# Performance work log

Measured on AMD Instinct MI355X. Metric: run time of the kernel, lower is better.

Reference implementation:

```python
import jax, jax.numpy as jnp
import numpy as np
import math

D_MODEL = 1024
D_STATE = 16
D_CONV = 4
EXPAND = 2
D_INNER = EXPAND * D_MODEL
DT_RANK = 64
BATCH = 4
SEQ_LEN = 2048


def setup_inputs() -> dict:
    key = jax.random.key(0)
    ks = jax.random.split(key, 10)
    hidden_states = jax.random.normal(ks[0], (BATCH, SEQ_LEN, D_MODEL), jnp.float32)
    in_proj_w = jax.random.normal(ks[1], (D_MODEL, 2 * D_INNER), jnp.float32) * (D_MODEL ** -0.5)
    conv_w = jax.random.normal(ks[2], (D_INNER, D_CONV), jnp.float32) * (D_CONV ** -0.5)
    conv_b = jnp.zeros((D_INNER,), jnp.float32)
    x_proj_w = jax.random.normal(ks[3], (D_INNER, DT_RANK + 2 * D_STATE), jnp.float32) * (D_INNER ** -0.5)
    dt_init_std = DT_RANK ** -0.5
    dt_proj_w = jax.random.uniform(ks[4], (DT_RANK, D_INNER), jnp.float32, -dt_init_std, dt_init_std)
    # inverse-softplus init of dt bias: dt ~ logUniform(dt_min, dt_max)
    dt_min, dt_max, dt_floor = 0.001, 0.1, 1e-4
    dt = jnp.exp(jax.random.uniform(ks[5], (D_INNER,), jnp.float32) * (math.log(dt_max) - math.log(dt_min)) + math.log(dt_min))
    dt = jnp.clip(dt, dt_floor, None)
    dt_proj_b = dt + jnp.log(-jnp.expm1(-dt))
    A = jnp.tile(jnp.arange(1, D_STATE + 1, dtype=jnp.float32)[None, :], (D_INNER, 1))
    A_log = jnp.log(A)
    D = jnp.ones((D_INNER,), jnp.float32)
    out_proj_w = jax.random.normal(ks[6], (D_INNER, D_MODEL), jnp.float32) * (D_INNER ** -0.5)
    return {
        "hidden_states": hidden_states,
        "in_proj_w": in_proj_w,
        "conv_w": conv_w,
        "conv_b": conv_b,
        "x_proj_w": x_proj_w,
        "dt_proj_w": dt_proj_w,
        "dt_proj_b": dt_proj_b,
        "A_log": A_log,
        "D": D,
        "out_proj_w": out_proj_w,
    }


def _mamba_forward(hidden_states, in_proj_w, conv_w, conv_b, x_proj_w, dt_proj_w, dt_proj_b, A_log, D, out_proj_w):
    b, L, _ = hidden_states.shape
    d_state = A_log.shape[1]
    dt_rank = dt_proj_w.shape[0]
    K = conv_w.shape[1]

    xz = hidden_states @ in_proj_w                     # (b, L, 2*d_inner)
    x, z = jnp.split(xz, 2, axis=-1)                   # each (b, L, d_inner)

    # causal depthwise conv1d (padding = K-1, truncated to L)
    x_pad = jnp.pad(x, ((0, 0), (K - 1, 0), (0, 0)))
    x = sum(x_pad[:, k:k + L, :] * conv_w[:, k] for k in range(K)) + conv_b
    x = jax.nn.silu(x)

    x_dbl = x @ x_proj_w                               # (b, L, dt_rank + 2*d_state)
    dt, B, C = jnp.split(x_dbl, [dt_rank, dt_rank + d_state], axis=-1)
    dt = jax.nn.softplus(dt @ dt_proj_w + dt_proj_b)   # (b, L, d_inner)
    A = -jnp.exp(A_log)                                # (d_inner, d_state)

    def step(h, inp):
        x_t, dt_t, B_t, C_t = inp                      # (b,d), (b,d), (b,n), (b,n)
        dA = jnp.exp(A[None] * dt_t[..., None])        # (b, d, n)
        h = dA * h + dt_t[..., None] * B_t[:, None, :] * x_t[..., None]
        y_t = jnp.einsum('bdn,bn->bd', h, C_t) + D * x_t
        return h, y_t

    h0 = jnp.zeros((b, x.shape[-1], d_state), x.dtype)
    xs = (x.transpose(1, 0, 2), dt.transpose(1, 0, 2), B.transpose(1, 0, 2), C.transpose(1, 0, 2))
    _, ys = jax.lax.scan(step, h0, xs)                 # ys: (L, b, d_inner)
    y = ys.transpose(1, 0, 2) * jax.nn.silu(z)
    return y @ out_proj_w                              # (b, L, d_model)


def reference(hidden_states, in_proj_w, conv_w, conv_b, x_proj_w, dt_proj_w, dt_proj_b, A_log, D, out_proj_w):
    return _mamba_forward(hidden_states, in_proj_w, conv_w, conv_b, x_proj_w, dt_proj_w, dt_proj_b, A_log, D, out_proj_w)
```

## Files before the change

### kernel.cpp

```cpp
#include <hip/hip_runtime.h>
#include <hip/hip_bf16.h>


#define DM 1024
#define DS 16
#define DC 4
#define DI 2048
#define DR 64
#define NB 4
#define SL 2048
#define NTOK (NB*SL)
#define XDBL_W (DR + 2*DS)
#define CONV_R 8

typedef __hip_bfloat16 bf16;
typedef unsigned short u16;
typedef __attribute__((ext_vector_type(8))) short s8v;
typedef __attribute__((ext_vector_type(4))) float f4v;
typedef __attribute__((ext_vector_type(4))) unsigned short us4;

__device__ __forceinline__ float b2f(bf16 v) { return __bfloat162float(v); }
__device__ __forceinline__ bf16  f2b(float v) { return __float2bfloat16(v); }
__device__ __forceinline__ u16 f2u(float x) {
    union { bf16 h; u16 s; } u; u.h = f2b(x); return u.s;
}
__device__ __forceinline__ float u2f(u16 s) {
    union { bf16 h; u16 s; } u; u.s = s; return b2f(u.h);
}

__device__ __forceinline__ bool sniff_bf16(const void* Dones) {
    return ((const u16*)Dones)[0] == 0x3F80u;
}

__device__ __forceinline__ float softplus_fast(float v) {
    return fmaxf(v, 0.f) + __logf(1.f + __expf(-fabsf(v)));
}

template<int MODE>
__device__ __forceinline__ float ld(const void* p, size_t i, bool bf) {
    if (MODE == 0) return b2f(((const bf16*)p)[i]);
    if (MODE == 1) return ((const float*)p)[i];
    return bf ? b2f(((const bf16*)p)[i]) : ((const float*)p)[i];
}
template<int MODE>
__device__ __forceinline__ void st(void* p, size_t i, bool bf, float v) {
    if (MODE == 0)      { ((bf16*)p)[i] = f2b(v); }
    else if (MODE == 1) { ((float*)p)[i] = v; }
    else { if (bf) ((bf16*)p)[i] = f2b(v); else ((float*)p)[i] = v; }
}

template<int CM>
__device__ __forceinline__ void cstore(void* C, void* C2, size_t m, int n,
                                       int ldc, bool bf, float v) {
    if (CM == 3) {
        if (n < DR) ((bf16*)C2)[m * DR + n] = f2b(v);
        else        ((float*)C)[m * (2 * DS) + (n - DR)] = v;
    } else {
        st<CM>(C, m * (size_t)ldc + n, bf, v);
    }
}

#define AS1 __attribute__((address_space(1)))
#define AS3 __attribute__((address_space(3)))
__device__ __forceinline__ void gload_lds16(const void* g, void* l) {
    __builtin_amdgcn_global_load_lds((const AS1 unsigned int*)g,
                                     (AS3 unsigned int*)l, 16, 0, 0);
}

__global__ __launch_bounds__(256) void cast_bf16_kernel(
    const void* __restrict__ src, bf16* __restrict__ dst,
    const void* __restrict__ sniff)
{
    const bool bf = sniff_bf16(sniff);
    const size_t i = ((size_t)blockIdx.x * 256 + threadIdx.x) * 4;
    if (bf) {
        *(us4*)((u16*)dst + i) = *(const us4*)((const u16*)src + i);
    } else {
        const f4v f = *(const f4v*)((const float*)src + i);
        us4 o; o.x = f2u(f.x); o.y = f2u(f.y); o.z = f2u(f.z); o.w = f2u(f.w);
        *(us4*)((u16*)dst + i) = o;
    }
}

__global__ __launch_bounds__(256) void transpose_w(
    const void* __restrict__ w, bf16* __restrict__ wt,
    int K, int N, const void* __restrict__ sniff)
{
    const bool bf = sniff_bf16(sniff);
    __shared__ float t[32][33];
    const int tx = threadIdx.x & 31, ty = threadIdx.x >> 5;
    const int n0 = blockIdx.x * 32, k0 = blockIdx.y * 32;
    #pragma unroll
    for (int i = 0; i < 4; i++) {
        int k = k0 + ty + i * 8, n = n0 + tx;
        t[ty + i * 8][tx] = (n < N) ? ld<2>(w, (size_t)k * N + n, bf) : 0.f;
    }
    __syncthreads();
    #pragma unroll
    for (int i = 0; i < 4; i++) {
        int n = n0 + ty + i * 8, k = k0 + tx;
        wt[(size_t)n * K + k] = f2b(t[tx][ty + i * 8]);
    }
}

template<int BM, int BN, int WM, int WN, int CM>
__global__ __launch_bounds__(WM*WN*64, 2) void gemm_big(
    const bf16* __restrict__ A, int lda,
    const bf16* __restrict__ Bt,
    void* __restrict__ C, int ldc, int K,
    const void* __restrict__ sniff)
{
    constexpr int NT  = WM * WN;
    constexpr int NTH = NT * 64;
    constexpr int WAVE_M = BM / WM, WAVE_N = BN / WN;
    constexpr int MR = WAVE_M / 16, NR = WAVE_N / 16, MR2 = MR / 2;
    constexpr int CH_ROWS = NTH / 8;
    constexpr int ACH = BM / CH_ROWS;
    constexpr int BCH = BN / CH_ROWS;

    const bool bf = sniff_bf16(sniff);
    __shared__ short Asm[2][BM * 64];
    __shared__ short Bsm[2][BN * 64];

    const int tid = threadIdx.x, lane = tid & 63, wave = tid >> 6;
    const int wm = wave / WN, wn = wave % WN;
    const int ll = lane & 15, qd = lane >> 4;
    const int m0 = blockIdx.x * BM, n0 = blockIdx.y * BN;

    const int s_r  = tid >> 3;
    const int s_cb = ((tid & 7) * 16) ^ ((s_r & 7) << 4);

    const char* Ab = (const char*)A;
    const char* Bb = (const char*)Bt;

    f4v acc[MR][NR];
    #pragma unroll
    for (int i = 0; i < MR; i++)
        #pragma unroll
        for (int j = 0; j < NR; j++) acc[i][j] = (f4v){0.f, 0.f, 0.f, 0.f};

    #pragma unroll
    for (int c = 0; c < ACH; c++)
        gload_lds16(Ab + (((size_t)(m0 + c * CH_ROWS + s_r) * lda) << 1) + s_cb,
                    (char*)&Asm[0][0] + (c * NTH + tid) * 16);
    #pragma unroll
    for (int c = 0; c < BCH; c++)
        gload_lds16(Bb + (((size_t)(n0 + c * CH_ROWS + s_r) * K) << 1) + s_cb,
                    (char*)&Bsm[0][0] + (c * NTH + tid) * 16);
    asm volatile("s_waitcnt vmcnt(0)" ::: "memory");
    __builtin_amdgcn_sched_barrier(0);
    __builtin_amdgcn_s_barrier();

    const int NTILE = K >> 6;
    for (int t = 0; t < NTILE; ++t) {
        const int cur = t & 1, nxt = cur ^ 1;
        const int kk = (t + 1) << 6;
        const bool more = (t + 1 < NTILE);
        const char* Ac = (const char*)&Asm[cur][0];
        const char* Bc = (const char*)&Bsm[cur][0];
        #pragma unroll
        for (int p = 0; p < 4; ++p) {
            const int kh = p >> 1, mh = p & 1;
            const int kb = kh * 64;
            s8v af[MR2], bv[NR];
            #pragma unroll
            for (int i = 0; i < MR2; i++) {
                const int row = wm * WAVE_M + (mh * MR2 + i) * 16 + ll;
                af[i] = *(const s8v*)(Ac + (size_t)row * 128
                                        + ((kb + qd * 16) ^ ((ll & 7) << 4)));
            }
            #pragma unroll
            for (int j = 0; j < NR; j++) {
                const int row = wn * WAVE_N + j * 16 + ll;
                bv[j] = *(const s8v*)(Bc + (size_t)row * 128
                                        + ((kb + qd * 16) ^ ((ll & 7) << 4)));
            }
            if (p == 0 && more) {
                #pragma unroll
                for (int c = 0; c < ACH; c++)
                    gload_lds16(Ab + (((size_t)(m0 + c * CH_ROWS + s_r) * lda + kk) << 1) + s_cb,
                                (char*)&Asm[nxt][0] + (c * NTH + tid) * 16);
            }
            if (p == 1 && more) {
                #pragma unroll
                for (int c = 0; c < BCH; c++)
                    gload_lds16(Bb + (((size_t)(n0 + c * CH_ROWS + s_r) * K + kk) << 1) + s_cb,
                                (char*)&Bsm[nxt][0] + (c * NTH + tid) * 16);
            }
            __builtin_amdgcn_sched_barrier(0);
            __builtin_amdgcn_s_barrier();
            asm volatile("s_waitcnt lgkmcnt(0)" ::: "memory");
            __builtin_amdgcn_sched_barrier(0);
            __builtin_amdgcn_s_setprio(1);
            #pragma unroll
            for (int i = 0; i < MR2; i++)
                #pragma unroll
                for (int j = 0; j < NR; j++)
                    acc[mh * MR2 + i][j] = __builtin_amdgcn_mfma_f32_16x16x32_bf16(
                        af[i], bv[j], acc[mh * MR2 + i][j], 0, 0, 0);
            __builtin_amdgcn_s_setprio(0);
            if (p == 3) {
                asm volatile("s_waitcnt vmcnt(0)" ::: "memory");
            }
            __builtin_amdgcn_sched_barrier(0);
            __builtin_amdgcn_s_barrier();
        }
    }

    #pragma unroll
    for (int i = 0; i < MR; i++) {
        #pragma unroll
        for (int j = 0; j < NR; j++) {
            const int col = n0 + wn * WAVE_N + j * 16 + ll;
            #pragma unroll
            for (int r = 0; r < 4; r++) {
                const int row = m0 + wm * WAVE_M + i * 16 + qd * 4 + r;
                st<CM>(C, (size_t)row * ldc + col, bf, acc[i][j][r]);
            }
        }
    }
}

template<int CM, int EPI>
__global__ __launch_bounds__(256) void gemm_mfma(
    const bf16* __restrict__ A, int lda,
    const bf16* __restrict__ Bt,
    void* __restrict__ C, void* __restrict__ C2, int ldc,
    int M, int N, int K,
    const void* __restrict__ bias,
    const void* __restrict__ sniff)
{
    const bool bf = sniff_bf16(sniff);
    __shared__ short As[128 * 32];
    __shared__ short Bs[128 * 32];

    const int tid  = threadIdx.x;
    const int lane = tid & 63;
    const int wave = tid >> 6;
    const int wm = (wave & 1) * 64;
    const int wn = (wave >> 1) * 64;
    const int m0 = blockIdx.x * 128;
    const int n0 = blockIdx.y * 128;
    const int ll = lane & 15;
    const int qd = lane >> 4;

    const int srow  = lane >> 2;
    const int skoff = (lane & 3) * 8;

    const short* Ag = (const short*)A;
    const short* Bg = (const short*)Bt;
    char* AsB = (char*)As + wave * 2048 + lane * 16;
    char* BsB = (char*)Bs + wave * 2048 + lane * 16;
    const size_t a_row = (size_t)(m0 + wave * 32 + srow);
    const size_t b_row = (size_t)(n0 + wave * 32 + srow);

    f4v acc[4][4];
    #pragma unroll
    for (int i = 0; i < 4; i++)
        #pragma unroll
        for (int j = 0; j < 4; j++)
            acc[i][j] = (f4v){0.f, 0.f, 0.f, 0.f};

    for (int k0 = 0; k0 < K; k0 += 32) {
        gload_lds16(Ag + a_row * lda + k0 + skoff,            AsB);
        gload_lds16(Ag + (a_row + 16) * lda + k0 + skoff,     AsB + 1024);
        gload_lds16(Bg + b_row * K + k0 + skoff,              BsB);
        gload_lds16(Bg + (b_row + 16) * K + k0 + skoff,       BsB + 1024);
        __syncthreads();

        s8v af[4], bfr[4];
        #pragma unroll
        for (int s = 0; s < 4; s++)
            af[s] = *(const s8v*)&As[(wm + s * 16 + ll) * 32 + qd * 8];
        #pragma unroll
        for (int s = 0; s < 4; s++)
            bfr[s] = *(const s8v*)&Bs[(wn + s * 16 + ll) * 32 + qd * 8];
        #pragma unroll
        for (int i = 0; i < 4; i++)
            #pragma unroll
            for (int j = 0; j < 4; j++)
                acc[i][j] = __builtin_amdgcn_mfma_f32_16x16x32_bf16(
                    af[i], bfr[j], acc[i][j], 0, 0, 0);
        __syncthreads();
    }

    #pragma unroll
    for (int sn = 0; sn < 4; sn++) {
        const int cn = n0 + wn + sn * 16 + ll;
        if (cn >= N) continue;
        float bvv = 0.f;
        if (EPI == 1) bvv = ld<2>(bias, cn, bf);
        #pragma unroll
        for (int sm = 0; sm < 4; sm++) {
            #pragma unroll
            for (int r = 0; r < 4; r++) {
                const int cm = m0 + wm + sm * 16 + qd * 4 + r;
                float v = acc[sm][sn][r];
                if (EPI == 1) v = softplus_fast(v + bvv);
                cstore<CM>(C, C2, (size_t)cm, cn, ldc, bf, v);
            }
        }
    }
}

template<int AM, int CM, int EPI>
__global__ __launch_bounds__(256) void gemm_kernel(
    const void* __restrict__ A, int lda,
    const void* __restrict__ B, size_t bbase, int ldb,
    void* __restrict__ C, void* __restrict__ C2, int ldc,
    int M, int N, int K,
    const void* __restrict__ bias,
    const void* __restrict__ sniff)
{
    const bool bf = sniff_bf16(sniff);
    const int BM = 64, BN = 64, BK = 16;
    __shared__ float Asm[BK][BM + 4];
    __shared__ float Bsm[BK][BN + 4];

    const int tid = threadIdx.x;
    const int m0 = blockIdx.x * BM;
    const int n0 = blockIdx.y * BN;
    const int tx = tid % 16;
    const int ty = tid / 16;
    const int a_k = tid % BK;
    const int a_m = tid / BK;
    const int b_n = tid % BN;
    const int b_k = tid / BN;

    float acc[4][4] = {};

    for (int k0 = 0; k0 < K; k0 += BK) {
        #pragma unroll
        for (int i = 0; i < 4; i++) {
            int m = m0 + a_m + i * 16;
            float v = 0.f;
            if (m < M) v = ld<AM>(A, (size_t)m * lda + (k0 + a_k), bf);
            Asm[a_k][a_m + i * 16] = v;
        }
        #pragma unroll
        for (int i = 0; i < 4; i++) {
            int kk = b_k + i * 4;
            int n = n0 + b_n;
            float v = 0.f;
            if (n < N) v = ld<2>(B, bbase + (size_t)(k0 + kk) * ldb + n, bf);
            Bsm[kk][b_n] = v;
        }
        __syncthreads();
        #pragma unroll
        for (int kk = 0; kk < BK; kk++) {
            float av[4], bv[4];
            #pragma unroll
            for (int i = 0; i < 4; i++) av[i] = Asm[kk][ty * 4 + i];
            #pragma unroll
            for (int j = 0; j < 4; j++) bv[j] = Bsm[kk][tx * 4 + j];
            #pragma unroll
            for (int i = 0; i < 4; i++)
                #pragma unroll
                for (int j = 0; j < 4; j++)
                    acc[i][j] += av[i] * bv[j];
        }
        __syncthreads();
    }
    #pragma unroll
    for (int i = 0; i < 4; i++) {
        int m = m0 + ty * 4 + i;
        if (m >= M) continue;
        #pragma unroll
        for (int j = 0; j < 4; j++) {
            int n = n0 + tx * 4 + j;
            if (n >= N) continue;
            float v = acc[i][j];
            if (EPI == 1) {
                v += ld<2>(bias, n, bf);
                v = softplus_fast(v);
            }
            cstore<CM>(C, C2, (size_t)m, n, ldc, bf, v);
        }
    }
}

__global__ __launch_bounds__(256) void conv_silu_kernel(
    const bf16* __restrict__ xg, const void* __restrict__ w,
    const void* __restrict__ bias, bf16* __restrict__ xc,
    const void* __restrict__ sniff)
{
    const bool bf = sniff_bf16(sniff);
    const int c  = blockIdx.x * 256 + threadIdx.x;
    const int r0 = blockIdx.y * CONV_R;
    const int l0 = r0 % SL;

    float w0, w1, w2, w3;
    if (bf) {
        const us4 wv = *(const us4*)((const u16*)w + (size_t)c * 4);
        w0 = u2f(wv.x); w1 = u2f(wv.y); w2 = u2f(wv.z); w3 = u2f(wv.w);
    } else {
        const f4v wv = *(const f4v*)((const float*)w + (size_t)c * 4);
        w0 = wv.x; w1 = wv.y; w2 = wv.z; w3 = wv.w;
    }
    const float bs = ld<2>(bias, c, bf);

    float xm3 = (l0 >= 3) ? b2f(xg[(size_t)(r0 - 3) * DI + c]) : 0.f;
    float xm2 = (l0 >= 2) ? b2f(xg[(size_t)(r0 - 2) * DI + c]) : 0.f;
    float xm1 = (l0 >= 1) ? b2f(xg[(size_t)(r0 - 1) * DI + c]) : 0.f;

    #pragma unroll
    for (int i = 0; i < CONV_R; i++) {
        const size_t row = (size_t)(r0 + i);
        const float x0 = b2f(xg[row * DI + c]);
        const float acc = bs + w0 * xm3 + w1 * xm2 + w2 * xm1 + w3 * x0;
        const float s = acc / (1.f + __expf(-acc));
        xc[row * DI + c] = f2b(s);
        xm3 = xm2; xm2 = xm1; xm1 = x0;
    }
}

__global__ __launch_bounds__(256) void scan_pass1(
    const bf16* __restrict__ xc, const bf16* __restrict__ dt,
    const float* __restrict__ bc,
    const void* __restrict__ A_log, const void* __restrict__ Dones,
    float* __restrict__ P, float* __restrict__ Q, int nch)
{
    const bool bf = sniff_bf16(Dones);
    const int d = blockIdx.x * 256 + threadIdx.x;
    const int c = blockIdx.y;
    const int b = blockIdx.z;
    const int T = SL / nch;

    float a[DS], Pp[DS], Qq[DS];
    bool lad = true;
    #pragma unroll
    for (int n = 0; n < DS; n++) {
        a[n] = -__expf(ld<2>(A_log, (size_t)d * DS + n, bf));
        Pp[n] = 1.f; Qq[n] = 0.f;
        lad = lad && (fabsf(a[n] - (n + 1) * a[0]) < 1e-3f);
    }

    const size_t base = (size_t)b * SL + (size_t)c * T;
    if (lad) {
        const float a0 = a[0];
        for (int i = 0; i < T; i++) {
            const size_t row = base + i;
            const float xv  = b2f(xc[row * DI + d]);
            const float dtv = b2f(dt[row * DI + d]);
            const float dtx = dtv * xv;
            const float* Bv = bc + row * (2 * DS);
            const float r = __expf(a0 * dtv);
            float cur = r;
            #pragma unroll
            for (int n = 0; n < DS; n++) {
                Pp[n] *= cur;
                Qq[n] = cur * Qq[n] + dtx * Bv[n];
                cur *= r;
            }
        }
    } else {
        for (int i = 0; i < T; i++) {
            const size_t row = base + i;
            const float xv  = b2f(xc[row * DI + d]);
            const float dtv = b2f(dt[row * DI + d]);
            const float dtx = dtv * xv;
            const float* Bv = bc + row * (2 * DS);
            #pragma unroll
            for (int n = 0; n < DS; n++) {
                const float dA = __expf(a[n] * dtv);
                Pp[n] *= dA;
                Qq[n] = dA * Qq[n] + dtx * Bv[n];
            }
        }
    }
    const size_t o = (((size_t)b * nch + c) * DI + d) * DS;
    #pragma unroll
    for (int n = 0; n < DS; n++) { P[o + n] = Pp[n]; Q[o + n] = Qq[n]; }
}

__global__ __launch_bounds__(256) void scan_pass2(
    float* __restrict__ P, const float* __restrict__ Q, int nch)
{
    const int j = blockIdx.x * 256 + threadIdx.x;
    const int b = blockIdx.y;
    float h = 0.f;
    for (int c = 0; c < nch; c++) {
        const size_t o = ((size_t)b * nch + c) * (DI * DS) + j;
        const float p = P[o];
        const float q = Q[o];
        P[o] = h;
        h = p * h + q;
    }
}

__global__ __launch_bounds__(256) void scan_pass3(
    const bf16* __restrict__ xc, const bf16* __restrict__ dt,
    const float* __restrict__ bc, bf16* __restrict__ z,
    const void* __restrict__ A_log, const void* __restrict__ Dones,
    const float* __restrict__ H, int nch)
{
    const bool bf = sniff_bf16(Dones);
    const int d = blockIdx.x * 256 + threadIdx.x;
    const int c = blockIdx.y;
    const int b = blockIdx.z;
    const int T = SL / nch;

    float a[DS], h[DS];
    bool lad = true;
    const size_t o = (((size_t)b * nch + c) * DI + d) * DS;
    #pragma unroll
    for (int n = 0; n < DS; n++) {
        a[n] = -__expf(ld<2>(A_log, (size_t)d * DS + n, bf));
        h[n] = H[o + n];
        lad = lad && (fabsf(a[n] - (n + 1) * a[0]) < 1e-3f);
    }
    const float dD = ld<2>(Dones, d, bf);
    const size_t base = (size_t)b * SL + (size_t)c * T;

    if (lad) {
        const float a0 = a[0];
        for (int i = 0; i < T; i++) {
            const size_t row = base + i;
            const float xv  = b2f(xc[row * DI + d]);
            const float dtv = b2f(dt[row * DI + d]);
            const float zv  = b2f(z[row * DI + d]);
            const float dtx = dtv * xv;
            const float* Bv = bc + row * (2 * DS);
            const float* Cv = Bv + DS;
            const float r = __expf(a0 * dtv);
            float cur = r;
            float y = dD * xv;
            #pragma unroll
            for (int n = 0; n < DS; n++) {
                h[n] = cur * h[n] + dtx * Bv[n];
                y += h[n] * Cv[n];
                cur *= r;
            }
            const float g = zv / (1.f + __expf(-zv));
            z[row * DI + d] = f2b(y * g);
        }
    } else {
        for (int i = 0; i < T; i++) {
            const size_t row = base + i;
            const float xv  = b2f(xc[row * DI + d]);
            const float dtv = b2f(dt[row * DI + d]);
            const float zv  = b2f(z[row * DI + d]);
            const float dtx = dtv * xv;
            const float* Bv = bc + row * (2 * DS);
            const float* Cv = Bv + DS;
            float y = dD * xv;
            #pragma unroll
            for (int n = 0; n < DS; n++) {
                const float dA = __expf(a[n] * dtv);
                h[n] = dA * h[n] + dtx * Bv[n];
                y += h[n] * Cv[n];
            }
            const float g = zv / (1.f + __expf(-zv));
            z[row * DI + d] = f2b(y * g);
        }
    }
}

__global__ __launch_bounds__(256) void scan_serial(
    const bf16* __restrict__ xc, const bf16* __restrict__ dt,
    const float* __restrict__ bc, bf16* __restrict__ z,
    const void* __restrict__ A_log, const void* __restrict__ Dones)
{
    const bool bf = sniff_bf16(Dones);
    const int d = blockIdx.x * 256 + threadIdx.x;
    const int b = blockIdx.y;
    float a[DS], h[DS];
    #pragma unroll
    for (int n = 0; n < DS; n++) {
        a[n] = -__expf(ld<2>(A_log, (size_t)d * DS + n, bf));
        h[n] = 0.f;
    }
    const float dD = ld<2>(Dones, d, bf);
    const size_t base = (size_t)b * SL;
    for (int l = 0; l < SL; l++) {
        const size_t row = base + l;
        const float xv  = b2f(xc[row * DI + d]);
        const float dtv = b2f(dt[row * DI + d]);
        const float* Bv = bc + row * (2 * DS);
        const float dtx = dtv * xv;
        float y = dD * xv;
        #pragma unroll
        for (int n = 0; n < DS; n++) {
            const float dA = __expf(a[n] * dtv);
            h[n] = dA * h[n] + dtx * Bv[n];
            y += h[n] * Bv[DS + n];
        }
        const float zv = b2f(z[row * DI + d]);
        const float g = zv / (1.f + __expf(-zv));
        z[row * DI + d] = f2b(y * g);
    }
}

extern "C" void kernel_launch(void* const* d_in, const int* in_sizes, int n_in,
                              void* d_out, int out_size, void* d_ws, size_t ws_size,
                              hipStream_t stream) {
    const void* hs        = d_in[0];
    const void* in_proj_w = d_in[1];
    const void* conv_w    = d_in[2];
    const void* conv_b    = d_in[3];
    const void* x_proj_w  = d_in[4];
    const void* dt_proj_w = d_in[5];
    const void* dt_proj_b = d_in[6];
    const void* A_log     = d_in[7];
    const void* Dones     = d_in[8];
    const void* out_proj_w= d_in[9];

    char* ws = (char*)d_ws;
    bf16*  xg   = (bf16*)(ws);
    bf16*  xc   = (bf16*)(ws + 33554432);
    bf16*  hsb  = (bf16*)(ws + 33554432);
    bf16*  z    = (bf16*)(ws + 67108864);
    float* bc   = (float*)(ws + 100663296);
    bf16*  dtf  = (bf16*)(ws + 101711872);
    const size_t WT_OFF = 102760448;
    bf16* in_projT  = (bf16*)(ws + WT_OFF);
    bf16* x_projT   = (bf16*)(ws + WT_OFF);
    bf16* dt_projT  = (bf16*)(ws + WT_OFF + 524288);
    bf16* out_projT = (bf16*)(ws + WT_OFF);
    const bool mfma_ok = ws_size >= WT_OFF + 8388608;

    const size_t per_chunk = (size_t)NB * DI * DS * 4 * 2;
    int nch = 32;
    while (nch > 1 && WT_OFF + (size_t)nch * per_chunk > ws_size) nch >>= 1;
    const bool chunked = (WT_OFF + (size_t)nch * per_chunk <= ws_size);
    float* P = (float*)(ws + WT_OFF);
    float* Q = P + (size_t)NB * nch * DI * DS;

    bf16* dtb = xg;

    if (mfma_ok) {
        cast_bf16_kernel<<<(NTOK*DM/4)/256, 256, 0, stream>>>(hs, hsb, Dones);
        transpose_w<<<dim3((2*DI)/32, DM/32), 256, 0, stream>>>(
            in_proj_w, in_projT, DM, 2*DI, Dones);
        gemm_big<256, 256, 2, 4, 0><<<dim3(NTOK/256, DI/256), 512, 0, stream>>>(
            hsb, DM, in_projT, xg, DI, DM, Dones);
        gemm_big<256, 256, 2, 4, 0><<<dim3(NTOK/256, DI/256), 512, 0, stream>>>(
            hsb, DM, in_projT + (size_t)DI * DM, z, DI, DM, Dones);
        conv_silu_kernel<<<dim3(DI/256, NTOK/CONV_R), 256, 0, stream>>>(
            xg, conv_w, conv_b, xc, Dones);
        transpose_w<<<dim3(128/32, DI/32), 256, 0, stream>>>(
            x_proj_w, x_projT, DI, XDBL_W, Dones);
        gemm_mfma<3, 0><<<dim3(NTOK/128, 1), 256, 0, stream>>>(
            xc, DI, x_projT, bc, dtf, 0, NTOK, XDBL_W, DI, nullptr, Dones);
        transpose_w<<<dim3(DI/32, DR/32), 256, 0, stream>>>(
            dt_proj_w, dt_projT, DR, DI, Dones);
        gemm_mfma<0, 1><<<dim3(NTOK/128, DI/128), 256, 0, stream>>>(
            dtf, DR, dt_projT, dtb, nullptr, DI, NTOK, DI, DR, dt_proj_b, Dones);
    } else {
        gemm_kernel<2, 0, 0><<<dim3(NTOK/64, DI/64), 256, 0, stream>>>(
            hs, DM, in_proj_w, 0, 2*DI, xg, nullptr, DI, NTOK, DI, DM, nullptr, Dones);
        gemm_kernel<2, 0, 0><<<dim3(NTOK/64, DI/64), 256, 0, stream>>>(
            hs, DM, in_proj_w, DI, 2*DI, z, nullptr, DI, NTOK, DI, DM, nullptr, Dones);
        conv_silu_kernel<<<dim3(DI/256, NTOK/CONV_R), 256, 0, stream>>>(
            xg, conv_w, conv_b, xc, Dones);
        gemm_kernel<0, 3, 0><<<dim3(NTOK/64, (XDBL_W + 63)/64), 256, 0, stream>>>(
            xc, DI, x_proj_w, 0, XDBL_W, bc, dtf, 0, NTOK, XDBL_W, DI, nullptr, Dones);
        gemm_kernel<0, 0, 1><<<dim3(NTOK/64, DI/64), 256, 0, stream>>>(
            dtf, DR, dt_proj_w, 0, DI, dtb, nullptr, DI, NTOK, DI, DR, dt_proj_b, Dones);
    }

    if (chunked) {
        scan_pass1<<<dim3(DI/256, nch, NB), 256, 0, stream>>>(
            xc, dtb, bc, A_log, Dones, P, Q, nch);
        scan_pass2<<<dim3((DI*DS)/256, NB), 256, 0, stream>>>(P, Q, nch);
        scan_pass3<<<dim3(DI/256, nch, NB), 256, 0, stream>>>(
            xc, dtb, bc, z, A_log, Dones, P, nch);
    } else {
        scan_serial<<<dim3(DI/256, NB), 256, 0, stream>>>(
            xc, dtb, bc, z, A_log, Dones);
    }

    if (mfma_ok) {
        transpose_w<<<dim3(DM/32, DI/32), 256, 0, stream>>>(
            out_proj_w, out_projT, DI, DM, Dones);
        gemm_big<256, 128, 4, 2, 2><<<dim3(NTOK/256, DM/128), 512, 0, stream>>>(
            z, DI, out_projT, d_out, DM, DI, Dones);
    } else {
        gemm_kernel<0, 2, 0><<<dim3(NTOK/64, DM/64), 256, 0, stream>>>(
            z, DI, out_proj_w, 0, DM, d_out, nullptr, DM, NTOK, DM, DI, nullptr, Dones);
    }
}
```

Before: 464.3 us.

## Stage B/C in shared memory and transpose chunk-state layout in chunked scan

Both chunked scan passes now copy the chunk's B/C rows into shared memory once per block instead of every thread reading them from global memory. The P/Q/H chunk-state layout is switched to state-major so the per-thread stores and loads coalesce across d. The geometric-decay recurrence is split into four independent multiplier chains, with partial output accumulators, to shorten dependency chains. P is now computed once from the chunk's total decay instead of every step. The fixed 64-row shared buffer assumes chunk length T is at most 64.

```diff
diff --git a/kernel.cpp b/kernel.cpp
--- a/kernel.cpp
+++ b/kernel.cpp
@@ -425,52 +425,76 @@
     const int c = blockIdx.y;
     const int b = blockIdx.z;
     const int T = SL / nch;
-
-    float a[DS], Pp[DS], Qq[DS];
+    __shared__ float bcs[64 * 2 * DS];
+
+    const size_t base = (size_t)b * SL + (size_t)c * T;
+    for (int k = threadIdx.x; k < T * 2 * DS; k += 256)
+        bcs[k] = bc[base * (2 * DS) + k];
+
+    float a[DS], Qq[DS];
     bool lad = true;
     #pragma unroll
     for (int n = 0; n < DS; n++) {
         a[n] = -__expf(ld<2>(A_log, (size_t)d * DS + n, bf));
-        Pp[n] = 1.f; Qq[n] = 0.f;
+        Qq[n] = 0.f;
         lad = lad && (fabsf(a[n] - (n + 1) * a[0]) < 1e-3f);
     }
-
-    const size_t base = (size_t)b * SL + (size_t)c * T;
+    __syncthreads();
+
+    const u16* xp = (const u16*)xc + base * DI + d;
+    const u16* tp = (const u16*)dt + base * DI + d;
+
+    float Pp[DS];
     if (lad) {
         const float a0 = a[0];
+        float R = 1.f;
         for (int i = 0; i < T; i++) {
-            const size_t row = base + i;
-            const float xv  = b2f(xc[row * DI + d]);
-            const float dtv = b2f(dt[row * DI + d]);
-            const float dtx = dtv * xv;
-            const float* Bv = bc + row * (2 * DS);
-            const float r = __expf(a0 * dtv);
-            float cur = r;
+            const float xv = u2f(xp[(size_t)i * DI]);
+            const float tv = u2f(tp[(size_t)i * DI]);
+            const float dtx = tv * xv;
+            const float* Bv = &bcs[i * 2 * DS];
+            const float r = __expf(a0 * tv);
+            const float r2 = r * r, r3 = r2 * r, r4 = r2 * r2;
+            float ca = r, cb = r2, cc = r3, cd = r4;
+            R *= r;
+            #pragma unroll
+            for (int n = 0; n < DS; n += 4) {
+                Qq[n]     = ca * Qq[n]     + dtx * Bv[n];
+                Qq[n + 1] = cb * Qq[n + 1] + dtx * Bv[n + 1];
+                Qq[n + 2] = cc * Qq[n + 2] + dtx * Bv[n + 2];
+                Qq[n + 3] = cd * Qq[n + 3] + dtx * Bv[n + 3];
+                ca *= r4; cb *= r4; cc *= r4; cd *= r4;
+            }
+        }
+        const float R2 = R * R, R3 = R2 * R, R4 = R2 * R2;
+        float pa = R, pb = R2, pc = R3, pd = R4;
+        #pragma unroll
+        for (int n = 0; n < DS; n += 4) {
+            Pp[n] = pa; Pp[n + 1] = pb; Pp[n + 2] = pc; Pp[n + 3] = pd;
+            pa *= R4; pb *= R4; pc *= R4; pd *= R4;
+        }
+    } else {
+        #pragma unroll
+        for (int n = 0; n < DS; n++) Pp[n] = 1.f;
+        for (int i = 0; i < T; i++) {
+            const float xv = u2f(xp[(size_t)i * DI]);
+            const float tv = u2f(tp[(size_t)i * DI]);
+            const float dtx = tv * xv;
+            const float* Bv = &bcs[i * 2 * DS];
             #pragma unroll
             for (int n = 0; n < DS; n++) {
-                Pp[n] *= cur;
-                Qq[n] = cur * Qq[n] + dtx * Bv[n];
-                cur *= r;
-            }
-        }
-    } else {
-        for (int i = 0; i < T; i++) {
-            const size_t row = base + i;
-            const float xv  = b2f(xc[row * DI + d]);
-            const float dtv = b2f(dt[row * DI + d]);
-            const float dtx = dtv * xv;
-            const float* Bv = bc + row * (2 * DS);
-            #pragma unroll
-            for (int n = 0; n < DS; n++) {
-                const float dA = __expf(a[n] * dtv);
+                const float dA = __expf(a[n] * tv);
                 Pp[n] *= dA;
                 Qq[n] = dA * Qq[n] + dtx * Bv[n];
             }
         }
     }
-    const size_t o = (((size_t)b * nch + c) * DI + d) * DS;
-    #pragma unroll
-    for (int n = 0; n < DS; n++) { P[o + n] = Pp[n]; Q[o + n] = Qq[n]; }
+    const size_t ob = ((size_t)b * nch + c) * (DS * DI) + d;
+    #pragma unroll
+    for (int n = 0; n < DS; n++) {
+        P[ob + (size_t)n * DI] = Pp[n];
+        Q[ob + (size_t)n * DI] = Qq[n];
+    }
 }
 
 __global__ __launch_bounds__(256) void scan_pass2(
@@ -499,59 +523,70 @@
     const int c = blockIdx.y;
     const int b = blockIdx.z;
     const int T = SL / nch;
+    __shared__ float bcs[64 * 2 * DS];
+
+    const size_t base = (size_t)b * SL + (size_t)c * T;
+    for (int k = threadIdx.x; k < T * 2 * DS; k += 256)
+        bcs[k] = bc[base * (2 * DS) + k];
 
     float a[DS], h[DS];
     bool lad = true;
-    const size_t o = (((size_t)b * nch + c) * DI + d) * DS;
+    const size_t ob = ((size_t)b * nch + c) * (DS * DI) + d;
     #pragma unroll
     for (int n = 0; n < DS; n++) {
         a[n] = -__expf(ld<2>(A_log, (size_t)d * DS + n, bf));
-        h[n] = H[o + n];
+        h[n] = H[ob + (size_t)n * DI];
         lad = lad && (fabsf(a[n] - (n + 1) * a[0]) < 1e-3f);
     }
     const float dD = ld<2>(Dones, d, bf);
-    const size_t base = (size_t)b * SL + (size_t)c * T;
+    __syncthreads();
+
+    const u16* xp = (const u16*)xc + base * DI + d;
+    const u16* tp = (const u16*)dt + base * DI + d;
+    u16*       zp = (u16*)z + base * DI + d;
 
     if (lad) {
         const float a0 = a[0];
         for (int i = 0; i < T; i++) {
-            const size_t row = base + i;
-            const float xv  = b2f(xc[row * DI + d]);
-            const float dtv = b2f(dt[row * DI + d]);
-            const float zv  = b2f(z[row * DI + d]);
-            const float dtx = dtv * xv;
-            const float* Bv = bc + row * (2 * DS);
+            const float xv = u2f(xp[(size_t)i * DI]);
+            const float tv = u2f(tp[(size_t)i * DI]);
+            const float zv = u2f(zp[(size_t)i * DI]);
+            const float dtx = tv * xv;
+            const float* Bv = &bcs[i * 2 * DS];
             const float* Cv = Bv + DS;
-            const float r = __expf(a0 * dtv);
-            float cur = r;
-            float y = dD * xv;
-            #pragma unroll
-            for (int n = 0; n < DS; n++) {
-                h[n] = cur * h[n] + dtx * Bv[n];
-                y += h[n] * Cv[n];
-                cur *= r;
-            }
+            const float r = __expf(a0 * tv);
+            const float r2 = r * r, r3 = r2 * r, r4 = r2 * r2;
+            float ca = r, cb = r2, cc = r3, cd = r4;
+            float ya = dD * xv, yb = 0.f, yc = 0.f, yd = 0.f;
+            #pragma unroll
+            for (int n = 0; n < DS; n += 4) {
+                h[n]     = ca * h[n]     + dtx * Bv[n];     ya += h[n]     * Cv[n];
+                h[n + 1] = cb * h[n + 1] + dtx * Bv[n + 1]; yb += h[n + 1] * Cv[n + 1];
+                h[n + 2] = cc * h[n + 2] + dtx * Bv[n + 2]; yc += h[n + 2] * Cv[n + 2];
+                h[n + 3] = cd * h[n + 3] + dtx * Bv[n + 3]; yd += h[n + 3] * Cv[n + 3];
+                ca *= r4; cb *= r4; cc *= r4; cd *= r4;
+            }
+            const float y = (ya + yb) + (yc + yd);
             const float g = zv / (1.f + __expf(-zv));
-            z[row * DI + d] = f2b(y * g);
+            zp[(size_t)i * DI] = f2u(y * g);
         }
     } else {
         for (int i = 0; i < T; i++) {
-            const size_t row = base + i;
-            const float xv  = b2f(xc[row * DI + d]);
-            const float dtv = b2f(dt[row * DI + d]);
-            const float zv  = b2f(z[row * DI + d]);
-            const float dtx = dtv * xv;
-            const float* Bv = bc + row * (2 * DS);
+            const float xv = u2f(xp[(size_t)i * DI]);
+            const float tv = u2f(tp[(size_t)i * DI]);
+            const float zv = u2f(zp[(size_t)i * DI]);
+            const float dtx = tv * xv;
+            const float* Bv = &bcs[i * 2 * DS];
             const float* Cv = Bv + DS;
             float y = dD * xv;
             #pragma unroll
             for (int n = 0; n < DS; n++) {
-                const float dA = __expf(a[n] * dtv);
+                const float dA = __expf(a[n] * tv);
                 h[n] = dA * h[n] + dtx * Bv[n];
                 y += h[n] * Cv[n];
             }
             const float g = zv / (1.f + __expf(-zv));
-            z[row * DI + d] = f2b(y * g);
+            zp[(size_t)i * DI] = f2u(y * g);
         }
     }
 }
```

Measured after the change: 469.9 us. Within noise of the previous version (+1.2%).
